# Kernel tuning notes

Measured on AMD Instinct MI355X. Metric: run time of the kernel, lower is better.

The kernel has to match this reference:

```python
import jax, jax.numpy as jnp
import numpy as np

N, DIM, HEADS, NS, KSP = 16384, 192, 6, 16, 16


def _forward(knn_idx, p, x, W_qkv, W_proj, b_proj, prop_W, prop_b, gA_W, gA_b, gB_W, gB_b,
             gC_W, gC_b, pos_W1, pos_b1, pos_gamma, pos_beta, pos_W2, pos_b2, kn,
             de_W1, de_b1, de_W2, de_b2, kp_W, kp_b, fus_W, fus_b):
    n, d = x.shape
    ns = knn_idx.shape[1]
    D = d // HEADS
    scale = D ** -0.5
    knn_xyz = p[knn_idx]                                  # [n,ns,3] irregular gather
    p_r = knn_xyz - p[:, None, :]                         # relative coords
    x_knn = x[knn_idx]                                    # [n,ns,d] irregular gather
    # PropagateLayer: rel-pos conditioned neighbor message + residual
    msg = jax.nn.relu(jnp.concatenate([x_knn, p_r], -1) @ prop_W + prop_b)
    x = x + msg.mean(1)
    # local polar representation
    dist_r = jnp.sqrt(jnp.sum(p_r * p_r, -1, keepdims=True) + 1e-12)   # [n,ns,1]
    geo_rep = jnp.concatenate([p_r, knn_xyz, jnp.broadcast_to(p[:, None, :], p_r.shape)], -1).mean(1)  # [n,9]
    geo_dis = dist_r.max(1)                               # [n,1]
    vol = (dist_r.mean() / (dist_r.max() + 1e-8)).reshape(1, 1)
    geo_rep = geo_rep @ gA_W + gA_b
    geo_dis = geo_dis @ gB_W + gB_b
    vol = vol @ gC_W + gC_b                               # [1,d] broadcast over n
    # keypoint distance features + attention pooling (KeyPointAttention)
    dist = jnp.sqrt(jnp.sum((p[:, None, :] - kn[None, :, :]) ** 2, -1) + 1e-12)  # [n,KSP]
    df = jax.nn.relu(dist[..., None] @ de_W1 + de_b1) @ de_W2 + de_b2            # [n,KSP,d]
    sc = jax.nn.softmax(df @ kp_W + kp_b, axis=1)
    dist_feat = (sc * df).sum(1)                          # [n,d]
    # FeatureFusion
    x = (x + geo_rep + geo_dis + vol + dist_feat) @ fus_W + fus_b
    # QueryGroup(local=True): window features + intra-window pairwise rel coords
    wx = x[knn_idx]                                       # [n,ns,d] irregular gather
    pos = (knn_xyz[:, None, :, :] - knn_xyz[:, :, None, :]).reshape(n, ns, ns * 3)  # [n,ns,48]

    def posi(i):  # Linear -> BatchNorm1d(dim) over (batch, window) -> ReLU -> Linear
        h = pos @ pos_W1[i] + pos_b1[i]                   # [n,ns,d]
        mu = h.mean((0, 1))
        var = h.var((0, 1))
        h = (h - mu) * jax.lax.rsqrt(var + 1e-5) * pos_gamma[i] + pos_beta[i]
        return jax.nn.relu(h) @ pos_W2[i] + pos_b2[i]

    pq, pk, pv = posi(0), posi(1), posi(2)
    q, k, v = jnp.split(wx @ W_qkv, 3, -1)

    def heads(t):
        return t.reshape(n, ns, HEADS, D).transpose(0, 2, 1, 3)  # [n,h,ns,D]

    q, k, v, pq, pk, pv = map(heads, (q, k, v, pq, pk, pv))
    dots = (jnp.einsum('nhid,nhjd->nhij', q, k)
            + jnp.einsum('nhid,nhjd->nhij', q, pq)
            + jnp.einsum('nhid,nhjd->nhij', k, pk))      # fused positional bias scores
    attn = jax.nn.softmax(dots * scale, -1)
    out = jnp.einsum('nhij,nhjd->nhid', attn, v + pv)
    out = out.transpose(0, 2, 1, 3).reshape(n, ns, d)[:, 0, :]   # take window center
    return out @ W_proj + b_proj


def setup_inputs() -> dict:
    key = jax.random.key(0)
    ks = jax.random.split(key, 20)
    d, s = DIM, 0.05
    rn = lambda i, shape: jax.random.normal(ks[i], shape, dtype=jnp.float32)
    return {
        'p': rn(0, (N, 3)),
        'x': rn(1, (N, d)),
        'knn_idx': jax.random.randint(ks[2], (N, NS), 0, N),
        'W_qkv': rn(3, (d, 3 * d)) * s,
        'W_proj': rn(4, (d, d)) * s,
        'b_proj': jnp.zeros((d,)),
        'prop_W': rn(5, (d + 3, d)) * s,
        'prop_b': jnp.zeros((d,)),
        'gA_W': rn(6, (9, d)) * s, 'gA_b': jnp.zeros((d,)),
        'gB_W': rn(7, (1, d)) * s, 'gB_b': jnp.zeros((d,)),
        'gC_W': rn(8, (1, d)) * s, 'gC_b': jnp.zeros((d,)),
        'pos_W1': rn(9, (3, NS * 3, d)) * s, 'pos_b1': jnp.zeros((3, d)),
        'pos_gamma': jnp.ones((3, d)), 'pos_beta': jnp.zeros((3, d)),
        'pos_W2': rn(10, (3, d, d)) * s, 'pos_b2': jnp.zeros((3, d)),
        'kn': rn(11, (KSP, 3)),
        'de_W1': rn(12, (1, d // 4)) * s, 'de_b1': jnp.zeros((d // 4,)),
        'de_W2': rn(13, (d // 4, d)) * s, 'de_b2': jnp.zeros((d,)),
        'kp_W': rn(14, (d, 1)) * s, 'kp_b': jnp.zeros((1,)),
        'fus_W': rn(15, (d, d)) * s, 'fus_b': jnp.zeros((d,)),
    }


def reference(p, x, knn_idx, W_qkv, W_proj, b_proj, prop_W, prop_b, gA_W, gA_b, gB_W, gB_b,
              gC_W, gC_b, pos_W1, pos_b1, pos_gamma, pos_beta, pos_W2, pos_b2, kn,
              de_W1, de_b1, de_W2, de_b2, kp_W, kp_b, fus_W, fus_b):
    return _forward(knn_idx, p, x, W_qkv, W_proj, b_proj, prop_W, prop_b, gA_W, gA_b,
                    gB_W, gB_b, gC_W, gC_b, pos_W1, pos_b1, pos_gamma, pos_beta,
                    pos_W2, pos_b2, kn, de_W1, de_b1, de_W2, de_b2, kp_W, kp_b, fus_W, fus_b)
```

## Files before the change

kernel.cpp:

```cpp
#include <hip/hip_runtime.h>
#include <math.h>

#define NP 16384
#define DD 192
#define NS 16
#define KSPN 16
#define MTOT (NP*NS)

typedef unsigned short ushort_t;
typedef __attribute__((ext_vector_type(8))) short short8;
typedef __attribute__((ext_vector_type(4))) float f32x4;

__device__ __forceinline__ ushort_t f2bf(float f) {
    union { float f; unsigned int u; } v; v.f = f;
    return (ushort_t)((v.u + 0x7FFFu + ((v.u >> 16) & 1u)) >> 16);
}
__device__ __forceinline__ float bf2f(ushort_t u) {
    return __uint_as_float(((unsigned int)u) << 16);
}

#define WS_KNN   0
#define WS_PR    (WS_KNN + NP*48)
#define WS_GEO9  (WS_PR + MTOT*3)
#define WS_GDIS  (WS_GEO9 + NP*9)
#define WS_STATS (WS_GDIS + NP)
#define WS_VOLV  (WS_STATS + 2512)
#define WS_AB    (WS_VOLV + DD)
#define WS_X1    (WS_AB + 1152)
#define WS_U     (WS_X1 + NP*DD)
#define WS_X2    (WS_U + NP*DD)
#define WS_QKV   (WS_X2 + NP*DD)
#define WS_SC    (WS_QKV + NP*576)
#define WS_ATTN  (WS_SC + NP*DD)
#define WS_W2T   (WS_ATTN + NP*96)
#define WS_PROPWT (WS_W2T + 36864)
#define WS_QKVT  (WS_PROPWT + 18432)
#define WS_FUSWT (WS_QKVT + 55296)
#define WS_PROJWT (WS_FUSWT + 18432)
#define WS_W1T   (WS_PROJWT + 18432)
#define WS_DEW2T (WS_W1T + 18432)
#define WS_XB    WS_SC
#define WS_UB    WS_ATTN
#define WS_X2B   WS_X2
#define WS_CTRB  WS_U

__global__ __launch_bounds__(256) void k_init(float* __restrict__ ws) {
    int t = blockIdx.x * 256 + threadIdx.x;
    if (t < 2512) ws[WS_STATS + t] = 0.f;
}

__global__ __launch_bounds__(256) void k_w2t(const float* __restrict__ posW2,
                                             float* __restrict__ ws) {
    int e = blockIdx.x*256 + threadIdx.x;
    int c = e / DD, kk = e - c*DD;
    ws[WS_W2T + e] = posW2[(size_t)(2*DD + kk)*DD + c];
}

__global__ __launch_bounds__(256) void k_prep(
    const float* __restrict__ propW, const float* __restrict__ Wqkv,
    const float* __restrict__ fusW, const float* __restrict__ Wproj,
    const float* __restrict__ posW1, const float* __restrict__ deW2,
    float* __restrict__ ws)
{
    int e = blockIdx.x*256 + threadIdx.x;
    ushort_t* pwt = (ushort_t*)(ws + WS_PROPWT);
    ushort_t* qkt = (ushort_t*)(ws + WS_QKVT);
    ushort_t* fwt = (ushort_t*)(ws + WS_FUSWT);
    ushort_t* pjt = (ushort_t*)(ws + WS_PROJWT);
    ushort_t* w1t = (ushort_t*)(ws + WS_W1T);
    ushort_t* dwt = (ushort_t*)(ws + WS_DEW2T);
    if (e < 36864) {
        int n = e/192, k = e - n*192;
        pwt[e] = f2bf(propW[(size_t)k*192 + n]);
    } else if (e < 147456) {
        int r = e - 36864; int n = r/192, k = r - n*192;
        qkt[r] = f2bf(Wqkv[(size_t)k*576 + n]);
    } else if (e < 184320) {
        int r = e - 147456; int n = r/192, k = r - n*192;
        fwt[r] = f2bf(fusW[(size_t)k*192 + n]);
    } else if (e < 221184) {
        int r = e - 184320; int n = r/192, k = r - n*192;
        pjt[r] = f2bf(Wproj[(size_t)k*192 + n]);
    } else if (e < 258048) {
        int r = e - 221184;
        int i = r / 12288, rem = r - i*12288;
        int n = rem / 64, k = rem - n*64;
        w1t[r] = (k < 48) ? f2bf(posW1[(size_t)(i*48 + k)*DD + n]) : (ushort_t)0;
    } else if (e < 270336) {
        int r = e - 258048;
        int n = r / 64, k = r - n*64;
        dwt[r] = (k < 48) ? f2bf(deW2[(size_t)k*DD + n]) : (ushort_t)0;
    }
}

__global__ __launch_bounds__(256) void k_castx(const float* __restrict__ x,
                                               float* __restrict__ ws) {
    int e = blockIdx.x*256 + threadIdx.x;
    ((ushort_t*)(ws + WS_XB))[e] = f2bf(x[e]);
}

__global__ __launch_bounds__(256) void k1a_geom(
    const float* __restrict__ p, const int* __restrict__ knn,
    float* __restrict__ ws)
{
    __shared__ float red[32];
    const int t = threadIdx.x;
    const int w = t >> 4, u = t & 15;
    const int n = blockIdx.x*16 + w;
    const int idx = knn[n*NS + u];
    const float X0 = p[idx*3+0], X1 = p[idx*3+1], X2 = p[idx*3+2];
    const float pn0 = p[n*3+0], pn1 = p[n*3+1], pn2 = p[n*3+2];
    ws[WS_KNN + (size_t)n*48 + u*3 + 0] = X0;
    ws[WS_KNN + (size_t)n*48 + u*3 + 1] = X1;
    ws[WS_KNN + (size_t)n*48 + u*3 + 2] = X2;
    const float dx = X0-pn0, dy = X1-pn1, dz = X2-pn2;
    ws[WS_PR + (size_t)(n*NS+u)*3 + 0] = dx;
    ws[WS_PR + (size_t)(n*NS+u)*3 + 1] = dy;
    ws[WS_PR + (size_t)(n*NS+u)*3 + 2] = dz;
    const float dist = sqrtf(dx*dx + dy*dy + dz*dz + 1e-12f);
    float dmx = dist, dsm = dist, S0 = X0, S1 = X1, S2 = X2;
    #pragma unroll
    for (int off = 1; off < 16; off <<= 1) {
        dmx = fmaxf(dmx, __shfl_xor(dmx, off, 16));
        dsm += __shfl_xor(dsm, off, 16);
        S0 += __shfl_xor(S0, off, 16);
        S1 += __shfl_xor(S1, off, 16);
        S2 += __shfl_xor(S2, off, 16);
    }
    if (u == 0) {
        ws[WS_GDIS + n] = dmx;
        float m0 = S0*(1.f/16.f), m1 = S1*(1.f/16.f), m2 = S2*(1.f/16.f);
        float* g = ws + WS_GEO9 + (size_t)n*9;
        g[0] = m0-pn0; g[1] = m1-pn1; g[2] = m2-pn2;
        g[3] = m0; g[4] = m1; g[5] = m2;
        g[6] = pn0; g[7] = pn1; g[8] = pn2;
        red[w] = dsm; red[16+w] = dmx;
    }
    __syncthreads();
    if (t == 0) {
        float ds = 0.f, dm = 0.f;
        #pragma unroll
        for (int i = 0; i < 16; ++i) { ds += red[i]; dm = fmaxf(dm, red[16+i]); }
        atomicAdd(&ws[WS_STATS + 0], ds);
        atomicMax((int*)(ws + WS_STATS + 1), __float_as_int(dm));
    }
}

__global__ __launch_bounds__(256) void k1b_stats(float* __restrict__ ws)
{
    __shared__ float Xs[128][48];
    __shared__ float Ss[128][3];
    __shared__ float a3p[9][16];
    const int t = threadIdx.x;
    const int c0 = blockIdx.x * 128;
    for (int e = t; e < 1536; e += 256) {
        int r = e/12, q = e%12;
        *(float4*)&Xs[r][q*4] = *(const float4*)(ws + WS_KNN + (size_t)(c0+r)*48 + q*4);
    }
    __syncthreads();
    if (t < 128) {
        float s0 = 0.f, s1 = 0.f, s2 = 0.f;
        #pragma unroll
        for (int j = 0; j < 16; ++j) { s0 += Xs[t][3*j]; s1 += Xs[t][3*j+1]; s2 += Xs[t][3*j+2]; }
        Ss[t][0] = s0; Ss[t][1] = s1; Ss[t][2] = s2;
    }
    __syncthreads();
    {
        float acc[9];
        #pragma unroll
        for (int q = 0; q < 9; ++q) acc[q] = 0.f;
        for (int i = 0; i < 128; ++i) {
            int e = t;
            #pragma unroll
            for (int q = 0; q < 9; ++q) {
                int a = e/48, b = e%48;
                acc[q] += Xs[i][a] * Xs[i][b];
                e += 256;
            }
        }
        int e = t;
        #pragma unroll
        for (int q = 0; q < 9; ++q) { atomicAdd(&ws[WS_STATS + 50 + e], acc[q]); e += 256; }
    }
    if (t < 144) {
        int a = t/3, d = t%3;
        float s = 0.f;
        for (int i = 0; i < 128; ++i) s += Xs[i][a] * Ss[i][d];
        atomicAdd(&ws[WS_STATS + 2354 + t], s);
    }
    if (t < 144) {
        int q = t >> 4, part = t & 15;
        int d = q/3, e2 = q%3;
        float s = 0.f;
        for (int i = part*8; i < part*8 + 8; ++i) {
            #pragma unroll
            for (int j = 0; j < 16; ++j) s += Xs[i][3*j+d] * Xs[i][3*j+e2];
        }
        a3p[q][part] = s;
    }
    if (t < 48) {
        float s = 0.f;
        for (int i = 0; i < 128; ++i) s += Xs[i][t];
        atomicAdd(&ws[WS_STATS + 2 + t], s);
    }
    if (t < 3) {
        float s = 0.f;
        for (int i = 0; i < 128; ++i) s += Ss[i][t];
        atomicAdd(&ws[WS_STATS + 2507 + t], s);
    }
    __syncthreads();
    if (t < 9) {
        float s = 0.f;
        #pragma unroll
        for (int i = 0; i < 16; ++i) s += a3p[t][i];
        atomicAdd(&ws[WS_STATS + 2498 + t], s);
    }
}

__global__ __launch_bounds__(256) void k2_fold(
    const float* __restrict__ posW1, const float* __restrict__ posB1,
    const float* __restrict__ gamma, const float* __restrict__ beta,
    const float* __restrict__ gCW, const float* __restrict__ gCb,
    float* __restrict__ ws)
{
    __shared__ float M2n[48][48];
    __shared__ float pmean[48];
    __shared__ float Wc[48][193];
    const int t = threadIdx.x;
    const int i = blockIdx.x;
    for (int e = t; e < 2304; e += 256) {
        int a = e/48, b = e%48, ad = a%3, bd = b%3;
        float v = 16.f*ws[WS_STATS + 50 + e]
                - ws[WS_STATS + 2354 + a*3 + bd]
                - ws[WS_STATS + 2354 + b*3 + ad]
                + ws[WS_STATS + 2498 + ad*3 + bd];
        M2n[a][b] = v * (1.f/(float)MTOT);
    }
    if (t < 48) pmean[t] = (16.f*ws[WS_STATS + 2 + t] - ws[WS_STATS + 2507 + t%3])
                           * (1.f/(float)MTOT);
    if (t < DD) {
        for (int k = 0; k < 48; ++k) Wc[k][t] = posW1[(size_t)(i*48 + k)*DD + t];
    }
    __syncthreads();
    if (i == 0 && t < DD) {
        float dsum = ws[WS_STATS + 0];
        float dmax = __int_as_float(((const int*)(ws + WS_STATS))[1]);
        float vol = (dsum * (1.f/(float)MTOT)) / (dmax + 1e-8f);
        ws[WS_VOLV + t] = vol * gCW[t] + gCb[t];
    }
    if (t < DD) {
        float mu0 = 0.f;
        #pragma unroll 8
        for (int k = 0; k < 48; ++k) mu0 += pmean[k] * Wc[k][t];
        float e2 = 0.f;
        for (int a2 = 0; a2 < 48; ++a2) {
            float inner = 0.f;
            #pragma unroll 8
            for (int b2 = 0; b2 < 48; ++b2) inner += M2n[a2][b2] * Wc[b2][t];
            e2 += Wc[a2][t] * inner;
        }
        float var = fmaxf(e2 - mu0*mu0, 0.f);
        float as = rsqrtf(var + 1e-5f) * gamma[i*DD + t];
        ws[WS_AB + i*DD + t]       = as;
        ws[WS_AB + 576 + i*DD + t] = beta[i*DD + t] - mu0 * as;
    }
}

__global__ __launch_bounds__(256) void k_prop_mfma(
    const float* __restrict__ x, const int* __restrict__ knn,
    const float* __restrict__ propW, const float* __restrict__ propB,
    float* __restrict__ ws)
{
    __shared__ ushort_t As[64*40];
    __shared__ ushort_t Bs[192*40];
    __shared__ float prs[64*3];
    __shared__ float W3[3*192];
    __shared__ int idx64[64];
    const int t = threadIdx.x;
    const int mbase = blockIdx.x * 64;
    const ushort_t* xb = (const ushort_t*)(ws + WS_XB);
    const ushort_t* pwt = (const ushort_t*)(ws + WS_PROPWT);
    if (t < 64) idx64[t] = knn[mbase + t];
    for (int e = t; e < 576; e += 256) W3[e] = propW[(size_t)(192 + e/192)*DD + (e % 192)];
    for (int e = t; e < 192; e += 256) prs[e] = ws[WS_PR + (size_t)mbase*3 + e];
    const int wave = t >> 6, lane = t & 63, m = lane & 15, quad = lane >> 4;
    f32x4 acc[12];
    #pragma unroll
    for (int nt = 0; nt < 12; ++nt) acc[nt] = (f32x4){0.f,0.f,0.f,0.f};
    for (int ks = 0; ks < 6; ++ks) {
        const int k0 = ks*32;
        __syncthreads();
        {   int r = t >> 2, seg = t & 3;
            *(uint4*)&As[r*40 + seg*8] = *(const uint4*)(xb + (size_t)idx64[r]*192 + k0 + seg*8);
        }
        for (int e = t; e < 768; e += 256) {
            int n = e >> 2, seg = e & 3;
            *(uint4*)&Bs[n*40 + seg*8] = *(const uint4*)(pwt + (size_t)n*192 + k0 + seg*8);
        }
        __syncthreads();
        short8 a = *(const short8*)&As[(wave*16 + m)*40 + quad*8];
        #pragma unroll
        for (int nt = 0; nt < 12; ++nt) {
            short8 b = *(const short8*)&Bs[(nt*16 + m)*40 + quad*8];
            acc[nt] = __builtin_amdgcn_mfma_f32_16x16x32_bf16(a, b, acc[nt], 0, 0, 0);
        }
    }
    const int n = blockIdx.x*4 + wave;
    #pragma unroll
    for (int nt = 0; nt < 12; ++nt) {
        int col = nt*16 + m;
        float bv = propB[col];
        float w0 = W3[col], w1 = W3[192 + col], w2 = W3[384 + col];
        float s = 0.f;
        #pragma unroll
        for (int reg = 0; reg < 4; ++reg) {
            int j = wave*16 + quad*4 + reg;
            float v = acc[nt][reg] + prs[j*3+0]*w0 + prs[j*3+1]*w1 + prs[j*3+2]*w2 + bv;
            s += fmaxf(v, 0.f);
        }
        s += __shfl_xor(s, 16);
        s += __shfl_xor(s, 32);
        if (quad == 0)
            ws[WS_X1 + (size_t)n*DD + col] = x[(size_t)n*DD + col] + s * (1.f/16.f);
    }
}

__global__ __launch_bounds__(256) void gemm_mfma(
    const ushort_t* __restrict__ A, const ushort_t* __restrict__ Bt,
    const float* __restrict__ bias, float* __restrict__ Cf,
    ushort_t* __restrict__ Cb, int N)
{
    __shared__ ushort_t As[64*40];
    __shared__ ushort_t Bs[64*40];
    const int t = threadIdx.x;
    const int wave = t >> 6, lane = t & 63, m = lane & 15, quad = lane >> 4;
    const int rowBase = blockIdx.x * 64, colBase = blockIdx.y * 64;
    f32x4 acc[4];
    #pragma unroll
    for (int nt = 0; nt < 4; ++nt) acc[nt] = (f32x4){0.f,0.f,0.f,0.f};
    for (int ks = 0; ks < 6; ++ks) {
        __syncthreads();
        {   int r = t >> 2, seg = t & 3;
            *(uint4*)&As[r*40 + seg*8] = *(const uint4*)(A + (size_t)(rowBase + r)*192 + ks*32 + seg*8);
            *(uint4*)&Bs[r*40 + seg*8] = *(const uint4*)(Bt + (size_t)(colBase + r)*192 + ks*32 + seg*8);
        }
        __syncthreads();
        short8 a = *(const short8*)&As[(wave*16 + m)*40 + quad*8];
        #pragma unroll
        for (int nt = 0; nt < 4; ++nt) {
            short8 b = *(const short8*)&Bs[(nt*16 + m)*40 + quad*8];
            acc[nt] = __builtin_amdgcn_mfma_f32_16x16x32_bf16(a, b, acc[nt], 0, 0, 0);
        }
    }
    #pragma unroll
    for (int nt = 0; nt < 4; ++nt) {
        int col = colBase + nt*16 + m;
        float bv = bias ? bias[col] : 0.f;
        #pragma unroll
        for (int reg = 0; reg < 4; ++reg) {
            int row = rowBase + wave*16 + quad*4 + reg;
            float v = acc[nt][reg] + bv;
            if (Cf) Cf[(size_t)row*N + col] = v;
            else    Cb[(size_t)row*N + col] = f2bf(v);
        }
    }
}

__global__ __launch_bounds__(256) void k3a(
    const float* __restrict__ p, const float* __restrict__ kn,
    const float* __restrict__ deW1, const float* __restrict__ deB1,
    const float* __restrict__ deB2, const float* __restrict__ kpW,
    const float* __restrict__ gAW, const float* __restrict__ gAb,
    const float* __restrict__ gBW, const float* __restrict__ gBb,
    float* __restrict__ ws)
{
    __shared__ ushort_t fb[128*72];
    __shared__ float kds[8][16];
    __shared__ float w1s[48], b1s[48];
    __shared__ float dfeat[8][192];
    ushort_t* ub = (ushort_t*)(ws + WS_UB);
    const int t = threadIdx.x;
    const int nb = blockIdx.x * 8;
    if (t < 48) { w1s[t] = deW1[t]; b1s[t] = deB1[t]; }
    if (t < 128) {
        int w = t >> 4, kp = t & 15;
        float dx = p[(nb+w)*3+0]-kn[kp*3+0];
        float dy = p[(nb+w)*3+1]-kn[kp*3+1];
        float dz = p[(nb+w)*3+2]-kn[kp*3+2];
        kds[w][kp] = sqrtf(dx*dx + dy*dy + dz*dz + 1e-12f);
    }
    __syncthreads();
    for (int e = t; e < 128*64; e += 256) {
        int j = e >> 6, k = e & 63;
        float v = (k < 48) ? fmaxf(kds[j>>4][j&15]*w1s[k] + b1s[k], 0.f) : 0.f;
        fb[j*72 + k] = f2bf(v);
    }
    __syncthreads();
    const int wave = t >> 6, lane = t & 63, m = lane & 15, quad = lane >> 4;
    const ushort_t* dwt = (const ushort_t*)(ws + WS_DEW2T);
    short8 afr[2][2];
    #pragma unroll
    for (int mt = 0; mt < 2; ++mt)
        #pragma unroll
        for (int ks = 0; ks < 2; ++ks)
            afr[mt][ks] = *(const short8*)&fb[((wave*2 + mt)*16 + m)*72 + ks*32 + quad*8];
    float df[2][12][4];
    float sc[2][4];
    #pragma unroll
    for (int mt = 0; mt < 2; ++mt)
        #pragma unroll
        for (int reg = 0; reg < 4; ++reg) sc[mt][reg] = 0.f;
    for (int nt = 0; nt < 12; ++nt) {
        f32x4 acc0 = (f32x4){0.f,0.f,0.f,0.f};
        f32x4 acc1 = (f32x4){0.f,0.f,0.f,0.f};
        #pragma unroll
        for (int ks = 0; ks < 2; ++ks) {
            short8 b = *(const short8*)(dwt + ((size_t)(nt*16 + m)*64 + ks*32 + quad*8));
            acc0 = __builtin_amdgcn_mfma_f32_16x16x32_bf16(afr[0][ks], b, acc0, 0, 0, 0);
            acc1 = __builtin_amdgcn_mfma_f32_16x16x32_bf16(afr[1][ks], b, acc1, 0, 0, 0);
        }
        int col = nt*16 + m;
        float b2 = deB2[col], kw = kpW[col];
        #pragma unroll
        for (int reg = 0; reg < 4; ++reg) {
            float d0 = acc0[reg] + b2, d1 = acc1[reg] + b2;
            df[0][nt][reg] = d0; df[1][nt][reg] = d1;
            sc[0][reg] += d0*kw; sc[1][reg] += d1*kw;
        }
    }
    #pragma unroll
    for (int mt = 0; mt < 2; ++mt)
        #pragma unroll
        for (int reg = 0; reg < 4; ++reg) {
            float v = sc[mt][reg];
            v += __shfl_xor(v, 1, 16); v += __shfl_xor(v, 2, 16);
            v += __shfl_xor(v, 4, 16); v += __shfl_xor(v, 8, 16);
            sc[mt][reg] = v;
        }
    float wgt[2][4];
    #pragma unroll
    for (int mt = 0; mt < 2; ++mt) {
        float mx = fmaxf(fmaxf(sc[mt][0], sc[mt][1]), fmaxf(sc[mt][2], sc[mt][3]));
        mx = fmaxf(mx, __shfl_xor(mx, 16));
        mx = fmaxf(mx, __shfl_xor(mx, 32));
        float sm = 0.f;
        #pragma unroll
        for (int reg = 0; reg < 4; ++reg) { wgt[mt][reg] = expf(sc[mt][reg] - mx); sm += wgt[mt][reg]; }
        sm += __shfl_xor(sm, 16);
        sm += __shfl_xor(sm, 32);
        float inv = 1.f / sm;
        #pragma unroll
        for (int reg = 0; reg < 4; ++reg) wgt[mt][reg] *= inv;
    }
    for (int nt = 0; nt < 12; ++nt) {
        int col = nt*16 + m;
        #pragma unroll
        for (int mt = 0; mt < 2; ++mt) {
            float s = 0.f;
            #pragma unroll
            for (int reg = 0; reg < 4; ++reg) s += wgt[mt][reg] * df[mt][nt][reg];
            s += __shfl_xor(s, 16);
            s += __shfl_xor(s, 32);
            if (quad == 0) dfeat[wave*2 + mt][col] = s;
        }
    }
    __syncthreads();
    if (t < DD) {
        for (int w = 0; w < 8; ++w) {
            int n = nb + w;
            float uval = ws[WS_X1 + (size_t)n*DD + t] + gAb[t] + gBb[t]
                       + ws[WS_VOLV + t] + dfeat[w][t];
            uval += ws[WS_GDIS + n] * gBW[t];
            #pragma unroll
            for (int kk = 0; kk < 9; ++kk) uval += ws[WS_GEO9 + (size_t)n*9 + kk] * gAW[kk*DD + t];
            ub[(size_t)n*DD + t] = f2bf(uval);
        }
    }
}

__global__ __launch_bounds__(256, 4) void k_attn_fused(
    const int* __restrict__ knn,
    const float* __restrict__ posW2, const float* __restrict__ posB2,
    float* __restrict__ ws)
{
    __shared__ ushort_t rqs[8*6*192];
    __shared__ float qk[8*192];
    __shared__ float scb[8*192];
    __shared__ float dqk[8*96];
    __shared__ float attns[8*96];
    __shared__ float Xl[8][48];
    __shared__ int idxs[128];
    const int t = threadIdx.x;
    const int nb = blockIdx.x * 8;
    ushort_t* ctrb = (ushort_t*)(ws + WS_CTRB);
    const ushort_t* qkvb = (const ushort_t*)(ws + WS_QKV);
    if (t < 128) idxs[t] = knn[(nb + (t >> 4))*NS + (t & 15)];
    for (int e = t; e < 384; e += 256) {
        int w = e/48, k = e%48;
        Xl[w][k] = ws[WS_KNN + (size_t)(nb+w)*48 + k];
    }
    __syncthreads();
    const int wave = t >> 6, lane = t & 63, m = lane & 15, quad = lane >> 4;
    short8 afr[2][2];
    #pragma unroll
    for (int mt = 0; mt < 2; ++mt) {
        const int w = wave*2 + mt;
        #pragma unroll
        for (int ks = 0; ks < 2; ++ks) {
            short8 v;
            #pragma unroll
            for (int e = 0; e < 8; ++e) {
                const int k = ks*32 + quad*8 + e;
                float f = (k < 48) ? (Xl[w][k] - Xl[w][m*3 + (k % 3)]) : 0.f;
                v[e] = (short)f2bf(f);
            }
            afr[mt][ks] = v;
        }
    }
    const ushort_t* w1t = (const ushort_t*)(ws + WS_W1T);
    for (int i = 0; i < 2; ++i) {
        __syncthreads();
        for (int e = t; e < 8*192; e += 256) {
            int w = e/192, c = e%192;
            qk[e] = bf2f(qkvb[(size_t)idxs[w*16]*576 + i*192 + c]);
        }
        __syncthreads();
        if (t < 192) {
            const float* Wrow = posW2 + (size_t)i*DD*DD + (size_t)t*DD;
            for (int h = 0; h < 6; ++h) {
                float4 wr[8];
                #pragma unroll
                for (int q = 0; q < 8; ++q) wr[q] = *(const float4*)(Wrow + h*32 + q*4);
                float a[8];
                #pragma unroll
                for (int w = 0; w < 8; ++w) a[w] = 0.f;
                #pragma unroll
                for (int q = 0; q < 8; ++q) {
                    #pragma unroll
                    for (int d = 0; d < 4; ++d) {
                        float wv = (&wr[q].x)[d];
                        int c = h*32 + q*4 + d;
                        #pragma unroll
                        for (int w = 0; w < 8; ++w) a[w] += wv * qk[w*192 + c];
                    }
                }
                #pragma unroll
                for (int w = 0; w < 8; ++w) rqs[(w*6 + h)*192 + t] = f2bf(a[w]);
            }
        }
        __syncthreads();
        float s[48];
        #pragma unroll
        for (int e = 0; e < 48; ++e) s[e] = 0.f;
        for (int nt = 0; nt < 12; ++nt) {
            f32x4 acc0 = (f32x4){0.f,0.f,0.f,0.f};
            f32x4 acc1 = (f32x4){0.f,0.f,0.f,0.f};
            #pragma unroll
            for (int ks = 0; ks < 2; ++ks) {
                short8 b = *(const short8*)(w1t + ((size_t)(i*192 + nt*16 + m)*64 + ks*32 + quad*8));
                acc0 = __builtin_amdgcn_mfma_f32_16x16x32_bf16(afr[0][ks], b, acc0, 0, 0, 0);
                acc1 = __builtin_amdgcn_mfma_f32_16x16x32_bf16(afr[1][ks], b, acc1, 0, 0, 0);
            }
            int kk = nt*16 + m;
            float as = ws[WS_AB + i*DD + kk];
            float bb = ws[WS_AB + 576 + i*DD + kk];
            float h0[4], h1[4];
            #pragma unroll
            for (int reg = 0; reg < 4; ++reg) {
                h0[reg] = fmaxf(acc0[reg]*as + bb, 0.f);
                h1[reg] = fmaxf(acc1[reg]*as + bb, 0.f);
            }
            #pragma unroll
            for (int h = 0; h < 6; ++h) {
                float r0 = bf2f(rqs[((wave*2 + 0)*6 + h)*192 + kk]);
                float r1 = bf2f(rqs[((wave*2 + 1)*6 + h)*192 + kk]);
                #pragma unroll
                for (int reg = 0; reg < 4; ++reg) {
                    s[reg*6 + h]      += h0[reg]*r0;
                    s[24 + reg*6 + h] += h1[reg]*r1;
                }
            }
        }
        #pragma unroll
        for (int e = 0; e < 48; ++e) {
            float v = s[e];
            v += __shfl_xor(v, 1, 16); v += __shfl_xor(v, 2, 16);
            v += __shfl_xor(v, 4, 16); v += __shfl_xor(v, 8, 16);
            s[e] = v;
        }
        if (m == 0) {
            #pragma unroll
            for (int mt = 0; mt < 2; ++mt)
                #pragma unroll
                for (int reg = 0; reg < 4; ++reg) {
                    int w = wave*2 + mt, j = quad*4 + reg;
                    #pragma unroll
                    for (int h = 0; h < 6; ++h)
                        scb[w*192 + i*96 + h*16 + j] = s[mt*24 + reg*6 + h];
                }
        }
    }
    {
        const int w = t >> 5, r = t & 31, j = r >> 1, half = r & 1;
        const ushort_t* krow = qkvb + (size_t)idxs[w*16 + j]*576 + 192 + half*96;
        const ushort_t* qrow = qkvb + (size_t)idxs[w*16]*576 + half*96;
        float hd[3] = {0.f, 0.f, 0.f};
        #pragma unroll
        for (int q = 0; q < 12; ++q) {
            uint4 kv = *(const uint4*)(krow + q*8);
            uint4 qv = *(const uint4*)(qrow + q*8);
            float sv = 0.f;
            #pragma unroll
            for (int d = 0; d < 4; ++d) {
                unsigned int ku = (&kv.x)[d], qu = (&qv.x)[d];
                sv += __uint_as_float(ku << 16) * __uint_as_float(qu << 16);
                sv += __uint_as_float(ku & 0xffff0000u) * __uint_as_float(qu & 0xffff0000u);
            }
            hd[q >> 2] += sv;
        }
        dqk[w*96 + (half*3+0)*16 + j] = hd[0];
        dqk[w*96 + (half*3+1)*16 + j] = hd[1];
        dqk[w*96 + (half*3+2)*16 + j] = hd[2];
    }
    __syncthreads();
    {
        const float scale = 0.17677669529663687f;
        #pragma unroll
        for (int c = 0; c < 3; ++c) {
            int e = c*256 + t;
            int row = e >> 4, j = e & 15, w = row / 6, h = row % 6;
            float z = (dqk[e] + scb[w*192 + h*16 + j] + scb[w*192 + 96 + h*16 + j]) * scale;
            float mx = z;
            #pragma unroll
            for (int off = 1; off < 16; off <<= 1) mx = fmaxf(mx, __shfl_xor(mx, off, 16));
            float ex = expf(z - mx);
            float sm = ex;
            #pragma unroll
            for (int off = 1; off < 16; off <<= 1) sm += __shfl_xor(sm, off, 16);
            attns[w*96 + h*16 + j] = ex / sm;
        }
    }
    __syncthreads();
    float ctr1[8];
    if (t < DD) {
        const int h = t >> 5;
        #pragma unroll
        for (int w = 0; w < 8; ++w) {
            float sv = 0.f;
            #pragma unroll
            for (int j = 0; j < NS; ++j)
                sv += attns[w*96 + h*16 + j] * bf2f(qkvb[(size_t)idxs[w*16 + j]*576 + 384 + t]);
            ctr1[w] = sv;
        }
    }
    {
        ushort_t* wsum = rqs;
        const int w0 = wave*2, w1 = wave*2 + 1;
        for (int nt = 0; nt < 12; ++nt) {
            f32x4 acc0 = (f32x4){0.f,0.f,0.f,0.f};
            f32x4 acc1 = (f32x4){0.f,0.f,0.f,0.f};
            #pragma unroll
            for (int ks = 0; ks < 2; ++ks) {
                short8 b = *(const short8*)(w1t + ((size_t)(2*192 + nt*16 + m)*64 + ks*32 + quad*8));
                acc0 = __builtin_amdgcn_mfma_f32_16x16x32_bf16(afr[0][ks], b, acc0, 0, 0, 0);
                acc1 = __builtin_amdgcn_mfma_f32_16x16x32_bf16(afr[1][ks], b, acc1, 0, 0, 0);
            }
            int kk = nt*16 + m;
            float as = ws[WS_AB + 2*DD + kk];
            float bb = ws[WS_AB + 576 + 2*DD + kk];
            float h0[4], h1[4];
            #pragma unroll
            for (int reg = 0; reg < 4; ++reg) {
                h0[reg] = fmaxf(acc0[reg]*as + bb, 0.f);
                h1[reg] = fmaxf(acc1[reg]*as + bb, 0.f);
            }
            #pragma unroll
            for (int h = 0; h < 6; ++h) {
                float p0 = 0.f, p1 = 0.f;
                #pragma unroll
                for (int reg = 0; reg < 4; ++reg) {
                    int j = quad*4 + reg;
                    p0 += attns[w0*96 + h*16 + j] * h0[reg];
                    p1 += attns[w1*96 + h*16 + j] * h1[reg];
                }
                p0 += __shfl_xor(p0, 16); p0 += __shfl_xor(p0, 32);
                p1 += __shfl_xor(p1, 16); p1 += __shfl_xor(p1, 32);
                if (quad == 0) {
                    wsum[(w0*6 + h)*192 + kk] = f2bf(p0);
                    wsum[(w1*6 + h)*192 + kk] = f2bf(p1);
                }
            }
        }
    }
    __syncthreads();
    if (t < DD) {
        const ushort_t* wsum = rqs;
        const int h = t >> 5;
        float pvacc[8];
        #pragma unroll
        for (int w = 0; w < 8; ++w) pvacc[w] = 0.f;
        const float* wrow = ws + WS_W2T + (size_t)t*DD;
        for (int k4 = 0; k4 < 48; ++k4) {
            float4 wv = *(const float4*)(wrow + k4*4);
            #pragma unroll
            for (int w = 0; w < 8; ++w) {
                const ushort_t* av = &wsum[(w*6 + h)*192 + k4*4];
                pvacc[w] += bf2f(av[0])*wv.x + bf2f(av[1])*wv.y
                          + bf2f(av[2])*wv.z + bf2f(av[3])*wv.w;
            }
        }
        float b2 = posB2[2*DD + t];
        #pragma unroll
        for (int w = 0; w < 8; ++w)
            ctrb[(size_t)(nb+w)*DD + t] = f2bf(ctr1[w] + pvacc[w] + b2);
    }
}

extern "C" void kernel_launch(void* const* d_in, const int* in_sizes, int n_in,
                              void* d_out, int out_size, void* d_ws, size_t ws_size,
                              hipStream_t stream)
{
    const float* p     = (const float*)d_in[0];
    const float* x     = (const float*)d_in[1];
    const int*   knn   = (const int*)  d_in[2];
    const float* Wqkv  = (const float*)d_in[3];
    const float* Wproj = (const float*)d_in[4];
    const float* bproj = (const float*)d_in[5];
    const float* propW = (const float*)d_in[6];
    const float* propB = (const float*)d_in[7];
    const float* gAW   = (const float*)d_in[8];
    const float* gAb   = (const float*)d_in[9];
    const float* gBW   = (const float*)d_in[10];
    const float* gBb   = (const float*)d_in[11];
    const float* gCW   = (const float*)d_in[12];
    const float* gCb   = (const float*)d_in[13];
    const float* posW1 = (const float*)d_in[14];
    const float* posB1 = (const float*)d_in[15];
    const float* gamma = (const float*)d_in[16];
    const float* beta  = (const float*)d_in[17];
    const float* posW2 = (const float*)d_in[18];
    const float* posB2 = (const float*)d_in[19];
    const float* kn    = (const float*)d_in[20];
    const float* deW1  = (const float*)d_in[21];
    const float* deB1  = (const float*)d_in[22];
    const float* deW2  = (const float*)d_in[23];
    const float* deB2  = (const float*)d_in[24];
    const float* kpW   = (const float*)d_in[25];
    const float* kpB   = (const float*)d_in[26];
    const float* fusW  = (const float*)d_in[27];
    const float* fusB  = (const float*)d_in[28];
    float* ws   = (float*)d_ws;
    float* outp = (float*)d_out;
    (void)kpB;

    hipLaunchKernelGGL(k_init, dim3(10), dim3(256), 0, stream, ws);
    hipLaunchKernelGGL(k_w2t, dim3(144), dim3(256), 0, stream, posW2, ws);
    hipLaunchKernelGGL(k_prep, dim3(1056), dim3(256), 0, stream,
                       propW, Wqkv, fusW, Wproj, posW1, deW2, ws);
    hipLaunchKernelGGL(k_castx, dim3(NP*DD/256), dim3(256), 0, stream, x, ws);
    hipLaunchKernelGGL(k1a_geom, dim3(NP/16), dim3(256), 0, stream, p, knn, ws);
    hipLaunchKernelGGL(k1b_stats, dim3(NP/128), dim3(256), 0, stream, ws);
    hipLaunchKernelGGL(k2_fold, dim3(3), dim3(256), 0, stream,
                       posW1, posB1, gamma, beta, gCW, gCb, ws);
    hipLaunchKernelGGL(k_prop_mfma, dim3(MTOT/64), dim3(256), 0, stream,
                       x, knn, propW, propB, ws);
    hipLaunchKernelGGL(k3a, dim3(NP/8), dim3(256), 0, stream,
                       p, kn, deW1, deB1, deB2, kpW, gAW, gAb, gBW, gBb, ws);
    hipLaunchKernelGGL(gemm_mfma, dim3(NP/64, 3), dim3(256), 0, stream,
                       (const ushort_t*)(ws + WS_UB), (const ushort_t*)(ws + WS_FUSWT),
                       fusB, (float*)nullptr, (ushort_t*)(ws + WS_X2B), DD);
    hipLaunchKernelGGL(gemm_mfma, dim3(NP/64, 9), dim3(256), 0, stream,
                       (const ushort_t*)(ws + WS_X2B), (const ushort_t*)(ws + WS_QKVT),
                       (const float*)nullptr, (float*)nullptr,
                       (ushort_t*)(ws + WS_QKV), 576);
    hipLaunchKernelGGL(k_attn_fused, dim3(NP/8), dim3(256), 0, stream,
                       knn, posW2, posB2, ws);
    hipLaunchKernelGGL(gemm_mfma, dim3(NP/64, 3), dim3(256), 0, stream,
                       (const ushort_t*)(ws + WS_CTRB), (const ushort_t*)(ws + WS_PROJWT),
                       bproj, outp, (ushort_t*)nullptr, DD);
}
```

Before: 611.1 us.

## Move posW2 projections in attention kernel onto bf16 MFMA

The two small per-window matmuls with pos_W2 inside the fused attention kernel (the query/key projection and the final value-side projection) ran as scalar FP32 loops on 192 threads. They now run as 16x16x32 bf16 MFMA instructions across all four waves, with only 8 of the 16 M rows holding real data. pos_W2 is pre-cast to bf16, and a transposed copy is made inside the prep kernel, which removes the separate transpose kernel. This cuts per-block ALU work and idle threads. The cost is extra bf16 rounding of weights and intermediates, plus half of each MFMA being wasted on padding rows.

```diff
diff --git a/kernel.cpp b/kernel.cpp
--- a/kernel.cpp
+++ b/kernel.cpp
@@ -43,24 +43,19 @@
 #define WS_UB    WS_ATTN
 #define WS_X2B   WS_X2
 #define WS_CTRB  WS_U
+#define WS_W2B   (WS_SC + NP*96)
+#define WS_W2T2B (WS_W2B + 36864)
 
 __global__ __launch_bounds__(256) void k_init(float* __restrict__ ws) {
     int t = blockIdx.x * 256 + threadIdx.x;
     if (t < 2512) ws[WS_STATS + t] = 0.f;
-}
-
-__global__ __launch_bounds__(256) void k_w2t(const float* __restrict__ posW2,
-                                             float* __restrict__ ws) {
-    int e = blockIdx.x*256 + threadIdx.x;
-    int c = e / DD, kk = e - c*DD;
-    ws[WS_W2T + e] = posW2[(size_t)(2*DD + kk)*DD + c];
 }
 
 __global__ __launch_bounds__(256) void k_prep(
     const float* __restrict__ propW, const float* __restrict__ Wqkv,
     const float* __restrict__ fusW, const float* __restrict__ Wproj,
     const float* __restrict__ posW1, const float* __restrict__ deW2,
-    float* __restrict__ ws)
+    const float* __restrict__ posW2, float* __restrict__ ws)
 {
     int e = blockIdx.x*256 + threadIdx.x;
     ushort_t* pwt = (ushort_t*)(ws + WS_PROPWT);
@@ -69,6 +64,8 @@
     ushort_t* pjt = (ushort_t*)(ws + WS_PROJWT);
     ushort_t* w1t = (ushort_t*)(ws + WS_W1T);
     ushort_t* dwt = (ushort_t*)(ws + WS_DEW2T);
+    ushort_t* w2b = (ushort_t*)(ws + WS_W2B);
+    ushort_t* w2t2b = (ushort_t*)(ws + WS_W2T2B);
     if (e < 36864) {
         int n = e/192, k = e - n*192;
         pwt[e] = f2bf(propW[(size_t)k*192 + n]);
@@ -90,6 +87,13 @@
         int r = e - 258048;
         int n = r / 64, k = r - n*64;
         dwt[r] = (k < 48) ? f2bf(deW2[(size_t)k*DD + n]) : (ushort_t)0;
+    } else if (e < 344064) {
+        int r = e - 270336;
+        w2b[r] = f2bf(posW2[r]);
+    } else if (e < 380928) {
+        int r = e - 344064;
+        int tr = r / 192, k = r - tr*192;
+        w2t2b[r] = f2bf(posW2[(size_t)2*36864 + (size_t)k*192 + tr]);
     }
 }
 
@@ -480,11 +484,11 @@
 
 __global__ __launch_bounds__(256, 4) void k_attn_fused(
     const int* __restrict__ knn,
-    const float* __restrict__ posW2, const float* __restrict__ posB2,
+    const float* __restrict__ posB2,
     float* __restrict__ ws)
 {
     __shared__ ushort_t rqs[8*6*192];
-    __shared__ float qk[8*192];
+    __shared__ ushort_t qkb[8*192];
     __shared__ float scb[8*192];
     __shared__ float dqk[8*96];
     __shared__ float attns[8*96];
@@ -493,7 +497,10 @@
     const int t = threadIdx.x;
     const int nb = blockIdx.x * 8;
     ushort_t* ctrb = (ushort_t*)(ws + WS_CTRB);
-    const ushort_t* qkvb = (const ushort_t*)(ws + WS_QKV);
+    const ushort_t* qkvb  = (const ushort_t*)(ws + WS_QKV);
+    const ushort_t* w2b   = (const ushort_t*)(ws + WS_W2B);
+    const ushort_t* w2t2b = (const ushort_t*)(ws + WS_W2T2B);
+    const ushort_t* w1t   = (const ushort_t*)(ws + WS_W1T);
     if (t < 128) idxs[t] = knn[(nb + (t >> 4))*NS + (t & 15)];
     for (int e = t; e < 384; e += 256) {
         int w = e/48, k = e%48;
@@ -517,35 +524,30 @@
             afr[mt][ks] = v;
         }
     }
-    const ushort_t* w1t = (const ushort_t*)(ws + WS_W1T);
     for (int i = 0; i < 2; ++i) {
         __syncthreads();
         for (int e = t; e < 8*192; e += 256) {
             int w = e/192, c = e%192;
-            qk[e] = bf2f(qkvb[(size_t)idxs[w*16]*576 + i*192 + c]);
+            qkb[e] = qkvb[(size_t)idxs[w*16]*576 + i*192 + c];
         }
         __syncthreads();
-        if (t < 192) {
-            const float* Wrow = posW2 + (size_t)i*DD*DD + (size_t)t*DD;
-            for (int h = 0; h < 6; ++h) {
-                float4 wr[8];
-                #pragma unroll
-                for (int q = 0; q < 8; ++q) wr[q] = *(const float4*)(Wrow + h*32 + q*4);
-                float a[8];
-                #pragma unroll
-                for (int w = 0; w < 8; ++w) a[w] = 0.f;
-                #pragma unroll
-                for (int q = 0; q < 8; ++q) {
+        #pragma unroll
+        for (int hh = 0; hh < 6; ++hh) {
+            short8 aq = *(const short8*)&qkb[(m & 7)*192 + hh*32 + quad*8];
+            #pragma unroll
+            for (int l = 0; l < 3; ++l) {
+                const int nt = wave*3 + l;
+                short8 b = *(const short8*)(w2b + (size_t)i*36864
+                            + (size_t)(nt*16 + m)*192 + hh*32 + quad*8);
+                f32x4 acc = (f32x4){0.f,0.f,0.f,0.f};
+                acc = __builtin_amdgcn_mfma_f32_16x16x32_bf16(aq, b, acc, 0, 0, 0);
+                if (quad < 2) {
                     #pragma unroll
-                    for (int d = 0; d < 4; ++d) {
-                        float wv = (&wr[q].x)[d];
-                        int c = h*32 + q*4 + d;
-                        #pragma unroll
-                        for (int w = 0; w < 8; ++w) a[w] += wv * qk[w*192 + c];
+                    for (int reg = 0; reg < 4; ++reg) {
+                        int w = quad*4 + reg;
+                        rqs[(w*6 + hh)*192 + nt*16 + m] = f2bf(acc[reg]);
                     }
                 }
-                #pragma unroll
-                for (int w = 0; w < 8; ++w) rqs[(w*6 + h)*192 + t] = f2bf(a[w]);
             }
         }
         __syncthreads();
@@ -693,26 +695,34 @@
         }
     }
     __syncthreads();
+    {
+        const ushort_t* wsum = rqs;
+        #pragma unroll
+        for (int l = 0; l < 3; ++l) {
+            const int nt = wave*3 + l;
+            const int h = nt >> 1;
+            f32x4 acc = (f32x4){0.f,0.f,0.f,0.f};
+            #pragma unroll
+            for (int ks = 0; ks < 6; ++ks) {
+                short8 a = *(const short8*)&wsum[((m & 7)*6 + h)*192 + ks*32 + quad*8];
+                short8 b = *(const short8*)(w2t2b + (size_t)(nt*16 + m)*192 + ks*32 + quad*8);
+                acc = __builtin_amdgcn_mfma_f32_16x16x32_bf16(a, b, acc, 0, 0, 0);
+            }
+            if (quad < 2) {
+                #pragma unroll
+                for (int reg = 0; reg < 4; ++reg) {
+                    int w = quad*4 + reg;
+                    scb[w*192 + nt*16 + m] = acc[reg];
+                }
+            }
+        }
+    }
+    __syncthreads();
     if (t < DD) {
-        const ushort_t* wsum = rqs;
-        const int h = t >> 5;
-        float pvacc[8];
-        #pragma unroll
-        for (int w = 0; w < 8; ++w) pvacc[w] = 0.f;
-        const float* wrow = ws + WS_W2T + (size_t)t*DD;
-        for (int k4 = 0; k4 < 48; ++k4) {
-            float4 wv = *(const float4*)(wrow + k4*4);
-            #pragma unroll
-            for (int w = 0; w < 8; ++w) {
-                const ushort_t* av = &wsum[(w*6 + h)*192 + k4*4];
-                pvacc[w] += bf2f(av[0])*wv.x + bf2f(av[1])*wv.y
-                          + bf2f(av[2])*wv.z + bf2f(av[3])*wv.w;
-            }
-        }
         float b2 = posB2[2*DD + t];
         #pragma unroll
         for (int w = 0; w < 8; ++w)
-            ctrb[(size_t)(nb+w)*DD + t] = f2bf(ctr1[w] + pvacc[w] + b2);
+            ctrb[(size_t)(nb+w)*DD + t] = f2bf(ctr1[w] + scb[w*192 + t] + b2);
     }
 }
 
@@ -754,9 +764,8 @@
     (void)kpB;
 
     hipLaunchKernelGGL(k_init, dim3(10), dim3(256), 0, stream, ws);
-    hipLaunchKernelGGL(k_w2t, dim3(144), dim3(256), 0, stream, posW2, ws);
-    hipLaunchKernelGGL(k_prep, dim3(1056), dim3(256), 0, stream,
-                       propW, Wqkv, fusW, Wproj, posW1, deW2, ws);
+    hipLaunchKernelGGL(k_prep, dim3(1488), dim3(256), 0, stream,
+                       propW, Wqkv, fusW, Wproj, posW1, deW2, posW2, ws);
     hipLaunchKernelGGL(k_castx, dim3(NP*DD/256), dim3(256), 0, stream, x, ws);
     hipLaunchKernelGGL(k1a_geom, dim3(NP/16), dim3(256), 0, stream, p, knn, ws);
     hipLaunchKernelGGL(k1b_stats, dim3(NP/128), dim3(256), 0, stream, ws);
@@ -774,7 +783,7 @@
                        (const float*)nullptr, (float*)nullptr,
                        (ushort_t*)(ws + WS_QKV), 576);
     hipLaunchKernelGGL(k_attn_fused, dim3(NP/8), dim3(256), 0, stream,
-                       knn, posW2, posB2, ws);
+                       knn, posB2, ws);
     hipLaunchKernelGGL(gemm_mfma, dim3(NP/64, 3), dim3(256), 0, stream,
                        (const ushort_t*)(ws + WS_CTRB), (const ushort_t*)(ws + WS_PROJWT),
                        bproj, outp, (ushort_t*)nullptr, DD);
```

Result: faster. 578.0 us (-5.4%).
